# Kernel optimization log

Hardware: AMD Instinct MI355X
Metric: run time of the kernel (lower is better)

The kernel has to match this reference:

```python
import jax, jax.numpy as jnp
import numpy as np

# Model dims (match init_kwargs)
B, H, W, C = 16, 6, 4096, 128
OVERLAP, NUM_PVQS, NUM_RVQS = 4, 3, 6
CB_DIM, CB_SIZE = 8, 1024
FIX = H * C                          # fix_dim = in_freq*in_dim = 768
HIDDEN = FIX * OVERLAP // NUM_PVQS   # 1024 per product group


def setup_inputs() -> dict:
    key = jax.random.key(0)
    k1, k2, k3, k4 = jax.random.split(key, 4)
    return {
        "z_e": jax.random.normal(k1, (B, H * W, C), jnp.float32),
        # per-(product-group, residual-stage) codebooks
        "embeds": jax.random.normal(k2, (NUM_PVQS, NUM_RVQS, CB_SIZE, CB_DIM), jnp.float32),
        # nn.Linear(hidden, codebook_dim, bias=False) stored as (hidden, cb_dim) so y = x @ W
        "proj_down": jax.random.normal(k3, (NUM_PVQS, HIDDEN, CB_DIM), jnp.float32) * (HIDDEN ** -0.5),
        "proj_up": jax.random.normal(k4, (NUM_PVQS, CB_DIM, HIDDEN), jnp.float32) * (CB_DIM ** -0.5),
        "num_streams": 6,
    }


def _l2n(x, eps=1e-12):
    return x / jnp.maximum(jnp.linalg.norm(x, axis=-1, keepdims=True), eps)


def _codebook(residual, embed):
    """One VQ codebook (l2norm variant): cdist + argmin + lookup + ST estimator.
    residual: (B, T, d); embed: (K, d)."""
    z = _l2n(residual)
    e = _l2n(embed)
    # squared euclidean distances (B, T, K)
    d = (z * z).sum(-1, keepdims=True) - 2.0 * jnp.einsum('btd,kd->btk', z, e) + (e * e).sum(-1)
    code = jnp.argmin(d, axis=-1)                      # (B, T) int
    q = jnp.take(e, code, axis=0)                      # (B, T, d)
    cb_loss = jnp.mean((q - jax.lax.stop_gradient(residual)) ** 2)
    cm_loss = jnp.mean((residual - jax.lax.stop_gradient(q)) ** 2)
    z_q = residual + jax.lax.stop_gradient(q - residual)   # straight-through
    return z_q, code, cb_loss, cm_loss


def reference(z_e, embeds, proj_down, proj_up, num_streams):
    # pre_process (dims=3): 'b (h w) c -> b w (c h)' then fold overlap frames
    x = z_e.reshape(B, H, W, C).transpose(0, 2, 3, 1).reshape(B, W, FIX)
    T = W // OVERLAP
    x = x.reshape(B, T, OVERLAP * FIX)

    zq_parts, code_parts = [], []
    cb_loss = 0.0
    cm_loss = 0.0
    for m in range(NUM_PVQS):
        xm = x[..., m * HIDDEN:(m + 1) * HIDDEN]
        residual = xm @ proj_down[m]                   # (B, T, CB_DIM)
        zq_m = jnp.zeros_like(residual)
        codes_m = []
        for i in range(num_streams):                   # residual VQ stages
            qi, ci, cb, cm = _codebook(residual, embeds[m, i])
            residual = residual - qi
            zq_m = zq_m + qi
            codes_m.append(ci)
            cb_loss = cb_loss + cb
            cm_loss = cm_loss + cm
        zq_parts.append(zq_m @ proj_up[m])             # (B, T, HIDDEN)
        code_parts.append(jnp.stack(codes_m, axis=1))  # (B, num_streams, T)

    zq = jnp.concatenate(zq_parts, axis=-1)            # (B, T, OVERLAP*FIX)
    codes = jnp.stack(code_parts, axis=2)              # (B, num_streams, num_pvqs, T)

    # post_process (dims=3): unfold overlap, 'b w (c h) -> b (h w) c'
    zq = zq.reshape(B, W, FIX).reshape(B, W, C, H).transpose(0, 3, 1, 2).reshape(B, H * W, C)
    return zq, codes, cb_loss / NUM_PVQS, cm_loss / NUM_PVQS
```

## Files before the change

### kernel.cpp

```cpp
#include <hip/hip_runtime.h>

#define BB        16
#define HH        6
#define WW        4096
#define CC        128
#define TT        1024
#define NTOK      16384
#define FIX       768
#define HID       1024
#define CBK       1024
#define CBD       8
#define NPVQ      3
#define NRVQ      6
#define ZQ_SIZE   50331648ull

#define OFF_ACC   0ull
#define OFF_EN    16ull
#define OFF_R     (OFF_EN + 1179648ull)
#define OFF_ZQ    (OFF_R + 3145728ull)

__global__ __launch_bounds__(256) void knorm(const float* __restrict__ emb,
                                             double* __restrict__ en) {
    int gid = blockIdx.x * 256 + threadIdx.x;
    if (gid >= NPVQ * NRVQ * CBK) return;
    const float* e = emb + (size_t)gid * CBD;
    double v[CBD];
    double s = 0.0;
#pragma unroll
    for (int d = 0; d < CBD; ++d) { v[d] = (double)e[d]; s += v[d] * v[d]; }
    double n = fmax(sqrt(s), 1e-12);
#pragma unroll
    for (int d = 0; d < CBD; ++d) en[(size_t)gid * CBD + d] = v[d] / n;
}

__global__ __launch_bounds__(256) void kproj(const float* __restrict__ ze,
                                             const float* __restrict__ pd,
                                             double* __restrict__ r_ws) {
    __shared__ float x[NPVQ * HID];
    const int tok = blockIdx.x;
    const int b = tok >> 10, t = tok & 1023;
    const int tid = threadIdx.x;
    const size_t zbase = (size_t)b * (HH * WW * CC);
#pragma unroll
    for (int q = 0; q < 12; ++q) {
        int idx = tid + 256 * q;
        int h = idx >> 9, rem = idx & 511, o = rem >> 7, c = rem & 127;
        float v = ze[zbase + (size_t)(h * WW + t * 4 + o) * CC + c];
        x[o * FIX + c * HH + h] = v;
    }
    __syncthreads();
    const int w = tid >> 6, l = tid & 63;
    if (w < NPVQ) {
        const int m = w;
        double acc[CBD] = {0, 0, 0, 0, 0, 0, 0, 0};
        for (int q = 0; q < 16; ++q) {
            int j = l + 64 * q;
            double xv = (double)x[m * HID + j];
            const float* pr = pd + (size_t)(m * HID + j) * CBD;
#pragma unroll
            for (int d = 0; d < CBD; ++d) acc[d] = fma(xv, (double)pr[d], acc[d]);
        }
#pragma unroll
        for (int off = 32; off >= 1; off >>= 1) {
#pragma unroll
            for (int d = 0; d < CBD; ++d) acc[d] += __shfl_down(acc[d], off, 64);
        }
        if (l == 0) {
            double* rp = r_ws + ((size_t)m * NTOK + tok) * CBD;
#pragma unroll
            for (int d = 0; d < CBD; ++d) rp[d] = acc[d];
        }
    }
}

#define KV_WAVES   8
#define KV_THREADS (KV_WAVES * 64)
#define KV_HALF    512
#define KV_WSLICE  (KV_HALF / KV_WAVES)

__global__ __launch_bounds__(KV_THREADS) void kvq(const double* __restrict__ en_all,
                                                  const double* __restrict__ r_ws,
                                                  float* __restrict__ zq_ws,
                                                  float* __restrict__ out,
                                                  const int* __restrict__ nsp,
                                                  double* __restrict__ accum) {
    __shared__ __align__(16) double tbl[KV_HALF * CBD];
    __shared__ double lds_d[KV_THREADS];
    __shared__ int    lds_k[KV_THREADS];

    const int blk = blockIdx.x;
    const int m = blk >> 8, g = blk & 255;
    const int tid = threadIdx.x;
    const int w = tid >> 6, l = tid & 63;
    const int tok = g * 64 + l;
    const int b = tok >> 10, t = tok & 1023;
    const int ns = *nsp;

    double r[CBD];
    {
        const double* rp = r_ws + ((size_t)m * NTOK + tok) * CBD;
#pragma unroll
        for (int d = 0; d < CBD; ++d) r[d] = rp[d];
    }
    double zq[CBD] = {0, 0, 0, 0, 0, 0, 0, 0};
    double loss = 0.0;

    const int kl0 = w * KV_WSLICE;
    for (int i = 0; i < ns; ++i) {
        const double* en = en_all + ((size_t)(m * NRVQ + i)) * CBK * CBD;
        double best = -1e300;
        int bk = 0;
#pragma unroll
        for (int p = 0; p < 2; ++p) {
            __syncthreads();
            {
                const float4* src = (const float4*)(en + (size_t)p * KV_HALF * CBD);
                float4* dst = (float4*)tbl;
#pragma unroll
                for (int q = 0; q < 4; ++q) dst[tid + KV_THREADS * q] = src[tid + KV_THREADS * q];
            }
            __syncthreads();
            const int kg0 = p * KV_HALF;
            for (int k = kl0; k < kl0 + KV_WSLICE; k += 4) {
                double dots[4];
#pragma unroll
                for (int u = 0; u < 4; ++u) {
                    const double* ev = tbl + (size_t)(k + u) * CBD;
                    double a0 = 0.0, a1 = 0.0;
#pragma unroll
                    for (int d = 0; d < CBD; d += 2) {
                        a0 = fma(r[d], ev[d], a0);
                        a1 = fma(r[d + 1], ev[d + 1], a1);
                    }
                    dots[u] = a0 + a1;
                }
#pragma unroll
                for (int u = 0; u < 4; ++u) {
                    if (dots[u] > best) { best = dots[u]; bk = kg0 + k + u; }
                }
            }
        }
        lds_d[tid] = best;
        lds_k[tid] = bk;
        __syncthreads();
        double bb = lds_d[l];
        int bbk = lds_k[l];
#pragma unroll
        for (int w2 = 1; w2 < KV_WAVES; ++w2) {
            double d2 = lds_d[w2 * 64 + l];
            int    k2 = lds_k[w2 * 64 + l];
            if (d2 > bb || (d2 == bb && k2 < bbk)) { bb = d2; bbk = k2; }
        }
        const double* qv = en + (size_t)bbk * CBD;
        if (w == 0) {
            double ls = 0.0;
#pragma unroll
            for (int d = 0; d < CBD; ++d) { double df = qv[d] - r[d]; ls += df * df; }
            loss += ls;
            out[ZQ_SIZE + ((size_t)(b * ns + i) * NPVQ + m) * TT + t] = (float)bbk;
        }
#pragma unroll
        for (int d = 0; d < CBD; ++d) { double q = qv[d]; r[d] -= q; zq[d] += q; }
    }

    if (w == 0) {
        float* zp = zq_ws + ((size_t)m * NTOK + tok) * CBD;
#pragma unroll
        for (int d = 0; d < CBD; ++d) zp[d] = (float)zq[d];
#pragma unroll
        for (int off = 32; off >= 1; off >>= 1) loss += __shfl_down(loss, off, 64);
        if (l == 0) atomicAdd(accum, loss);
    }
}

__global__ __launch_bounds__(256) void kout(const float* __restrict__ pu,
                                            const float* __restrict__ zq_ws,
                                            float* __restrict__ out,
                                            const int* __restrict__ nsp,
                                            const double* __restrict__ accum) {
    __shared__ float zl[32][NPVQ][CBD];
    const int blk = blockIdx.x;
    const int tok0 = blk * 32;
    const int b = tok0 >> 10, t0 = tok0 & 1023;
    const int tid = threadIdx.x;
#pragma unroll
    for (int q = 0; q < 3; ++q) {
        int ii = tid + 256 * q;
        int mm = ii >> 8, rem = ii & 255, tt = rem >> 3, d = rem & 7;
        zl[tt][mm][d] = zq_ws[((size_t)mm * NTOK + tok0 + tt) * CBD + d];
    }
    __syncthreads();
    const size_t obase = (size_t)b * (HH * WW * CC);
#pragma unroll 2
    for (int q = 0; q < 12; ++q) {
        int idx = tid + 256 * q;
        int h = idx >> 9, rem = idx & 511, o = rem >> 7, c = rem & 127;
        int f = o * FIX + c * HH + h;
        int m = f >> 10, j = f & 1023;
        float pu8[CBD];
#pragma unroll
        for (int d = 0; d < CBD; ++d) pu8[d] = pu[((size_t)(m * CBD + d)) * HID + j];
        size_t rowbase = obase + ((size_t)h * WW + t0 * 4 + o) * CC + c;
        for (int tt = 0; tt < 32; ++tt) {
            float y = 0.0f;
#pragma unroll
            for (int d = 0; d < CBD; ++d) y = fmaf(zl[tt][m][d], pu8[d], y);
            out[rowbase + (size_t)tt * 4 * CC] = y;
        }
    }
    if (blk == 0 && tid == 0) {
        int ns = *nsp;
        double s = *accum;
        float lv = (float)(s / (double)(NTOK * CBD * NPVQ));
        size_t lbase = ZQ_SIZE + (size_t)BB * ns * NPVQ * TT;
        out[lbase] = lv;
        out[lbase + 1] = lv;
    }
}

extern "C" void kernel_launch(void* const* d_in, const int* in_sizes, int n_in,
                              void* d_out, int out_size, void* d_ws, size_t ws_size,
                              hipStream_t stream) {
    const float* ze  = (const float*)d_in[0];
    const float* emb = (const float*)d_in[1];
    const float* pd  = (const float*)d_in[2];
    const float* pu  = (const float*)d_in[3];
    const int*   nsp = (const int*)d_in[4];
    float* out = (float*)d_out;
    char* ws = (char*)d_ws;

    double* accum = (double*)(ws + OFF_ACC);
    double* en    = (double*)(ws + OFF_EN);
    double* r_ws  = (double*)(ws + OFF_R);
    float*  zq_ws = (float*)(ws + OFF_ZQ);

    hipMemsetAsync(accum, 0, 16, stream);
    knorm<<<(NPVQ * NRVQ * CBK + 255) / 256, 256, 0, stream>>>(emb, en);
    kproj<<<NTOK, 256, 0, stream>>>(ze, pd, r_ws);
    kvq<<<NPVQ * (NTOK / 64), KV_THREADS, 0, stream>>>(en, r_ws, zq_ws, out, nsp, accum);
    kout<<<NTOK / 32, 256, 0, stream>>>(pu, zq_ws, out, nsp, accum);
}
```

Baseline: 386.8 us.

## Use fp32 codebook search with fp64 fallback, vectorize projection loads, transpose proj_up

The VQ argmax search now runs in fp32 against a float copy of the normalized codebook that fits whole in LDS. It tracks the top-two scores and falls back to an exact fp64 scan for tokens whose margin is below a small epsilon. The projection kernel handles two tokens per block with float4 loads and uses all six waves. proj_up is pre-transposed so the output kernel reads it with two float4 loads. The fp32 search cuts the fp64 FMA cost, but the epsilon must be large enough to keep argmin ties exact, and the fallback path diverges within a wave.

```diff
diff --git a/kernel.cpp b/kernel.cpp
--- a/kernel.cpp
+++ b/kernel.cpp
@@ -15,12 +15,15 @@
 #define ZQ_SIZE   50331648ull
 
 #define OFF_ACC   0ull
-#define OFF_EN    16ull
-#define OFF_R     (OFF_EN + 1179648ull)
+#define OFF_EN64  16ull
+#define OFF_EN32  (OFF_EN64 + 1179648ull)
+#define OFF_PUT   (OFF_EN32 + 589824ull)
+#define OFF_R     (OFF_PUT + 98304ull)
 #define OFF_ZQ    (OFF_R + 3145728ull)
 
 __global__ __launch_bounds__(256) void knorm(const float* __restrict__ emb,
-                                             double* __restrict__ en) {
+                                             double* __restrict__ en64,
+                                             float* __restrict__ en32) {
     int gid = blockIdx.x * 256 + threadIdx.x;
     if (gid >= NPVQ * NRVQ * CBK) return;
     const float* e = emb + (size_t)gid * CBD;
@@ -30,63 +33,83 @@
     for (int d = 0; d < CBD; ++d) { v[d] = (double)e[d]; s += v[d] * v[d]; }
     double n = fmax(sqrt(s), 1e-12);
 #pragma unroll
-    for (int d = 0; d < CBD; ++d) en[(size_t)gid * CBD + d] = v[d] / n;
-}
-
-__global__ __launch_bounds__(256) void kproj(const float* __restrict__ ze,
+    for (int d = 0; d < CBD; ++d) {
+        double q = v[d] / n;
+        en64[(size_t)gid * CBD + d] = q;
+        en32[(size_t)gid * CBD + d] = (float)q;
+    }
+}
+
+__global__ __launch_bounds__(256) void kputr(const float* __restrict__ pu,
+                                             float* __restrict__ pu_t) {
+    int gid = blockIdx.x * 256 + threadIdx.x;
+    if (gid >= NPVQ * CBD * HID) return;
+    int j = gid & (HID - 1), md = gid >> 10;
+    int m = md >> 3, d = md & 7;
+    pu_t[((size_t)m * HID + j) * CBD + d] = pu[gid];
+}
+
+__global__ __launch_bounds__(384) void kproj(const float* __restrict__ ze,
                                              const float* __restrict__ pd,
                                              double* __restrict__ r_ws) {
-    __shared__ float x[NPVQ * HID];
-    const int tok = blockIdx.x;
-    const int b = tok >> 10, t = tok & 1023;
+    __shared__ float x[2][NPVQ * HID];
+    const int tok0 = blockIdx.x * 2;
+    const int b = tok0 >> 10, t0 = tok0 & 1023;
     const int tid = threadIdx.x;
     const size_t zbase = (size_t)b * (HH * WW * CC);
 #pragma unroll
-    for (int q = 0; q < 12; ++q) {
-        int idx = tid + 256 * q;
-        int h = idx >> 9, rem = idx & 511, o = rem >> 7, c = rem & 127;
-        float v = ze[zbase + (size_t)(h * WW + t * 4 + o) * CC + c];
-        x[o * FIX + c * HH + h] = v;
+    for (int q = 0; q < 4; ++q) {
+        int g = tid + 384 * q;
+        int tk = g >= 768;
+        int gg = g - tk * 768;
+        int h = gg >> 7, v = gg & 127;
+        const float4 val = *(const float4*)(ze + zbase + (size_t)(h * WW + (t0 + tk) * 4) * CC + v * 4);
+        float vv[4] = {val.x, val.y, val.z, val.w};
+#pragma unroll
+        for (int e = 0; e < 4; ++e) {
+            int oc = v * 4 + e, o = oc >> 7, c = oc & 127;
+            x[tk][o * FIX + c * HH + h] = vv[e];
+        }
     }
     __syncthreads();
     const int w = tid >> 6, l = tid & 63;
-    if (w < NPVQ) {
-        const int m = w;
-        double acc[CBD] = {0, 0, 0, 0, 0, 0, 0, 0};
-        for (int q = 0; q < 16; ++q) {
-            int j = l + 64 * q;
-            double xv = (double)x[m * HID + j];
-            const float* pr = pd + (size_t)(m * HID + j) * CBD;
-#pragma unroll
-            for (int d = 0; d < CBD; ++d) acc[d] = fma(xv, (double)pr[d], acc[d]);
-        }
-#pragma unroll
-        for (int off = 32; off >= 1; off >>= 1) {
-#pragma unroll
-            for (int d = 0; d < CBD; ++d) acc[d] += __shfl_down(acc[d], off, 64);
-        }
-        if (l == 0) {
-            double* rp = r_ws + ((size_t)m * NTOK + tok) * CBD;
-#pragma unroll
-            for (int d = 0; d < CBD; ++d) rp[d] = acc[d];
-        }
+    const int tk = w >= 3, m = w - tk * 3;
+    double acc[CBD] = {0, 0, 0, 0, 0, 0, 0, 0};
+    for (int q = 0; q < 16; ++q) {
+        int j = l + 64 * q;
+        double xv = (double)x[tk][m * HID + j];
+        const float* pr = pd + (size_t)(m * HID + j) * CBD;
+#pragma unroll
+        for (int d = 0; d < CBD; ++d) acc[d] = fma(xv, (double)pr[d], acc[d]);
+    }
+#pragma unroll
+    for (int off = 32; off >= 1; off >>= 1) {
+#pragma unroll
+        for (int d = 0; d < CBD; ++d) acc[d] += __shfl_down(acc[d], off, 64);
+    }
+    if (l == 0) {
+        double* rp = r_ws + ((size_t)m * NTOK + tok0 + tk) * CBD;
+#pragma unroll
+        for (int d = 0; d < CBD; ++d) rp[d] = acc[d];
     }
 }
 
 #define KV_WAVES   8
 #define KV_THREADS (KV_WAVES * 64)
-#define KV_HALF    512
-#define KV_WSLICE  (KV_HALF / KV_WAVES)
+#define KV_WSLICE  (CBK / KV_WAVES)
+#define KV_EPS     5e-6f
 
 __global__ __launch_bounds__(KV_THREADS) void kvq(const double* __restrict__ en_all,
+                                                  const float* __restrict__ es_all,
                                                   const double* __restrict__ r_ws,
                                                   float* __restrict__ zq_ws,
                                                   float* __restrict__ out,
                                                   const int* __restrict__ nsp,
                                                   double* __restrict__ accum) {
-    __shared__ __align__(16) double tbl[KV_HALF * CBD];
-    __shared__ double lds_d[KV_THREADS];
-    __shared__ int    lds_k[KV_THREADS];
+    __shared__ __align__(16) float tbl[CBK * CBD];
+    __shared__ float mb1[KV_THREADS];
+    __shared__ float mb2[KV_THREADS];
+    __shared__ int   mbk[KV_THREADS];
 
     const int blk = blockIdx.x;
     const int m = blk >> 8, g = blk & 255;
@@ -108,48 +131,77 @@
     const int kl0 = w * KV_WSLICE;
     for (int i = 0; i < ns; ++i) {
         const double* en = en_all + ((size_t)(m * NRVQ + i)) * CBK * CBD;
-        double best = -1e300;
-        int bk = 0;
-#pragma unroll
-        for (int p = 0; p < 2; ++p) {
-            __syncthreads();
-            {
-                const float4* src = (const float4*)(en + (size_t)p * KV_HALF * CBD);
-                float4* dst = (float4*)tbl;
-#pragma unroll
-                for (int q = 0; q < 4; ++q) dst[tid + KV_THREADS * q] = src[tid + KV_THREADS * q];
+        const float*  es = es_all + ((size_t)(m * NRVQ + i)) * CBK * CBD;
+        double s = 0.0;
+#pragma unroll
+        for (int d = 0; d < CBD; ++d) s += r[d] * r[d];
+        double inv = 1.0 / fmax(sqrt(s), 1e-12);
+        float rn[CBD];
+#pragma unroll
+        for (int d = 0; d < CBD; ++d) rn[d] = (float)(r[d] * inv);
+
+        __syncthreads();
+        {
+            const float4* src = (const float4*)es;
+            float4* dst = (float4*)tbl;
+#pragma unroll
+            for (int q = 0; q < 4; ++q) dst[tid + KV_THREADS * q] = src[tid + KV_THREADS * q];
+        }
+        __syncthreads();
+
+        float b1 = -1e30f, b2 = -1e30f;
+        int bk = kl0;
+        for (int k = kl0; k < kl0 + KV_WSLICE; k += 4) {
+            float dots[4];
+#pragma unroll
+            for (int u = 0; u < 4; ++u) {
+                const float* ev = tbl + (size_t)(k + u) * CBD;
+                float a0 = 0.0f, a1 = 0.0f;
+#pragma unroll
+                for (int d = 0; d < CBD; d += 2) {
+                    a0 = fmaf(rn[d], ev[d], a0);
+                    a1 = fmaf(rn[d + 1], ev[d + 1], a1);
+                }
+                dots[u] = a0 + a1;
             }
-            __syncthreads();
-            const int kg0 = p * KV_HALF;
-            for (int k = kl0; k < kl0 + KV_WSLICE; k += 4) {
-                double dots[4];
-#pragma unroll
-                for (int u = 0; u < 4; ++u) {
-                    const double* ev = tbl + (size_t)(k + u) * CBD;
+#pragma unroll
+            for (int u = 0; u < 4; ++u) {
+                float dv = dots[u];
+                if (dv > b1) { b2 = b1; b1 = dv; bk = k + u; }
+                else if (dv > b2) { b2 = dv; }
+            }
+        }
+        mb1[tid] = b1; mb2[tid] = b2; mbk[tid] = bk;
+        __syncthreads();
+        float B1 = mb1[l], B2 = mb2[l];
+        int K = mbk[l];
+#pragma unroll
+        for (int w2 = 1; w2 < KV_WAVES; ++w2) {
+            float c1 = mb1[w2 * 64 + l];
+            float c2 = mb2[w2 * 64 + l];
+            int   ck = mbk[w2 * 64 + l];
+            if (c1 > B1) { B2 = fmaxf(B1, c2); B1 = c1; K = ck; }
+            else         { B2 = fmaxf(B2, c1); }
+        }
+        int bbk = K;
+        bool uncert = (B1 - B2) <= KV_EPS;
+        if (__any(uncert)) {
+            if (uncert) {
+                double best = -1e300;
+                int kk = 0;
+                for (int k = 0; k < CBK; ++k) {
+                    const double* ev = en + (size_t)k * CBD;
                     double a0 = 0.0, a1 = 0.0;
 #pragma unroll
                     for (int d = 0; d < CBD; d += 2) {
                         a0 = fma(r[d], ev[d], a0);
                         a1 = fma(r[d + 1], ev[d + 1], a1);
                     }
-                    dots[u] = a0 + a1;
+                    double dot = a0 + a1;
+                    if (dot > best) { best = dot; kk = k; }
                 }
-#pragma unroll
-                for (int u = 0; u < 4; ++u) {
-                    if (dots[u] > best) { best = dots[u]; bk = kg0 + k + u; }
-                }
+                bbk = kk;
             }
-        }
-        lds_d[tid] = best;
-        lds_k[tid] = bk;
-        __syncthreads();
-        double bb = lds_d[l];
-        int bbk = lds_k[l];
-#pragma unroll
-        for (int w2 = 1; w2 < KV_WAVES; ++w2) {
-            double d2 = lds_d[w2 * 64 + l];
-            int    k2 = lds_k[w2 * 64 + l];
-            if (d2 > bb || (d2 == bb && k2 < bbk)) { bb = d2; bbk = k2; }
         }
         const double* qv = en + (size_t)bbk * CBD;
         if (w == 0) {
@@ -173,7 +225,7 @@
     }
 }
 
-__global__ __launch_bounds__(256) void kout(const float* __restrict__ pu,
+__global__ __launch_bounds__(256) void kout(const float* __restrict__ pu_t,
                                             const float* __restrict__ zq_ws,
                                             float* __restrict__ out,
                                             const int* __restrict__ nsp,
@@ -197,9 +249,9 @@
         int h = idx >> 9, rem = idx & 511, o = rem >> 7, c = rem & 127;
         int f = o * FIX + c * HH + h;
         int m = f >> 10, j = f & 1023;
-        float pu8[CBD];
-#pragma unroll
-        for (int d = 0; d < CBD; ++d) pu8[d] = pu[((size_t)(m * CBD + d)) * HID + j];
+        const float4* p4 = (const float4*)(pu_t + ((size_t)m * HID + j) * CBD);
+        float4 pa = p4[0], pb = p4[1];
+        float pu8[CBD] = {pa.x, pa.y, pa.z, pa.w, pb.x, pb.y, pb.z, pb.w};
         size_t rowbase = obase + ((size_t)h * WW + t0 * 4 + o) * CC + c;
         for (int tt = 0; tt < 32; ++tt) {
             float y = 0.0f;
@@ -230,13 +282,16 @@
     char* ws = (char*)d_ws;
 
     double* accum = (double*)(ws + OFF_ACC);
-    double* en    = (double*)(ws + OFF_EN);
+    double* en64  = (double*)(ws + OFF_EN64);
+    float*  en32  = (float*)(ws + OFF_EN32);
+    float*  pu_t  = (float*)(ws + OFF_PUT);
     double* r_ws  = (double*)(ws + OFF_R);
     float*  zq_ws = (float*)(ws + OFF_ZQ);
 
     hipMemsetAsync(accum, 0, 16, stream);
-    knorm<<<(NPVQ * NRVQ * CBK + 255) / 256, 256, 0, stream>>>(emb, en);
-    kproj<<<NTOK, 256, 0, stream>>>(ze, pd, r_ws);
-    kvq<<<NPVQ * (NTOK / 64), KV_THREADS, 0, stream>>>(en, r_ws, zq_ws, out, nsp, accum);
-    kout<<<NTOK / 32, 256, 0, stream>>>(pu, zq_ws, out, nsp, accum);
-}
+    knorm<<<(NPVQ * NRVQ * CBK + 255) / 256, 256, 0, stream>>>(emb, en64, en32);
+    kputr<<<(NPVQ * CBD * HID + 255) / 256, 256, 0, stream>>>(pu, pu_t);
+    kproj<<<NTOK / 2, 384, 0, stream>>>(ze, pd, r_ws);
+    kvq<<<NPVQ * (NTOK / 64), KV_THREADS, 0, stream>>>(en64, en32, r_ws, zq_ws, out, nsp, accum);
+    kout<<<NTOK / 32, 256, 0, stream>>>(pu_t, zq_ws, out, nsp, accum);
+}
```

After: 473.0 us. 22.3% more time.
